# Optimization experiments

Hardware: AMD Instinct MI355X
Metric: run time of the kernel (lower is better)

The kernel has to match this reference:

```python
import jax, jax.numpy as jnp
import numpy as np

N = 25000   # num nodes
E = 500000  # num edges
B = 4       # num queries (batch)
D = 32      # hidden dim
R2 = 474    # doubled num_relation
L = 4       # num conv layers
EPS = 1e-6


def setup_inputs() -> dict:
    key = jax.random.key(0)
    ks = jax.random.split(key, 12)
    return {
        "node_in": jax.random.randint(ks[0], (E,), 0, N),
        "node_out": jax.random.randint(ks[1], (E,), 0, N),
        "relation": jax.random.randint(ks[2], (E,), 0, R2),
        "edge_weight": jnp.ones((E,), jnp.float32),
        "h_index": jax.random.randint(ks[3], (B,), 0, N),
        "r_index": jax.random.randint(ks[4], (B,), 0, R2),
        "query_embed": jax.random.normal(ks[5], (R2, D), jnp.float32) * 0.1,
        "rel_W": jax.random.normal(ks[6], (L, D, R2 * D), jnp.float32) * 0.05,
        "rel_b": jnp.zeros((L, R2 * D), jnp.float32),
        "lin_W": jax.random.normal(ks[7], (L, 13 * D, D), jnp.float32) * 0.05,
        "lin_b": jnp.zeros((L, D), jnp.float32),
        "mlp_W1": jax.random.normal(ks[8], (2 * D, 2 * D), jnp.float32) * 0.05,
        "mlp_b1": jnp.zeros((2 * D,), jnp.float32),
        "mlp_W2": jax.random.normal(ks[9], (2 * D, 1), jnp.float32) * 0.05,
        "mlp_b2": jnp.zeros((1,), jnp.float32),
    }


def _nbfnet(node_in, node_out, relation, h_index, r_index,
            edge_weight, query_embed, rel_W, rel_b, lin_W, lin_b,
            mlp_W1, mlp_b1, mlp_W2, mlp_b2):
    query = query_embed[r_index]                                   # [B, D]
    # boundary condition: query embedding placed at the head node of each query
    boundary = jnp.zeros((N, B, D), query.dtype).at[h_index, jnp.arange(B)].set(query)
    # append one self-entry per node (boundary message), as in the torch code
    node_out_ext = jnp.concatenate([node_out, jnp.arange(N)])      # [E+N]
    w_ext = jnp.concatenate([edge_weight, jnp.ones((N,), edge_weight.dtype)])[:, None, None]
    cnt = jax.ops.segment_sum(jnp.ones((E + N,), query.dtype), node_out_ext, N)[:, None, None]
    deg = jax.ops.segment_sum(edge_weight, node_out, N) + 1.0      # degree_out + 1, [N]
    scale = jnp.log(deg)
    scale = scale / scale.mean()
    scales = jnp.stack([jnp.ones_like(scale), scale, 1.0 / jnp.clip(scale, 0.01)], -1)  # [N,3]

    hidden = boundary
    for l in range(L):
        # dependent relation embeddings: [R2, B, D]
        rel_in = (query @ rel_W[l] + rel_b[l]).reshape(B, R2, D).transpose(1, 0, 2)
        # distmult message + boundary self-message: [E+N, B, D]
        msg = jnp.concatenate([rel_in[relation] * hidden[node_in], boundary], 0)
        mw = msg * w_ext
        mean = jax.ops.segment_sum(mw, node_out_ext, N) / cnt
        sq_mean = jax.ops.segment_sum(msg * mw, node_out_ext, N) / cnt
        mx = jax.ops.segment_max(mw, node_out_ext, N)
        mn = jax.ops.segment_min(mw, node_out_ext, N)
        std = jnp.sqrt(jnp.clip(sq_mean - mean * mean, EPS))
        feat = jnp.stack([mean, mx, mn, std], -1).reshape(N, B, 4 * D)   # PNA stats
        update = (feat[..., None] * scales[:, None, None, :]).reshape(N, B, 12 * D)
        hidden = jax.nn.relu(jnp.concatenate([hidden, update], -1) @ lin_W[l] + lin_b[l])

    feat = jnp.concatenate([hidden, jnp.broadcast_to(query[None], (N, B, D))], -1)  # [N,B,2D]
    h1 = jax.nn.relu(feat @ mlp_W1 + mlp_b1)
    score = (h1 @ mlp_W2 + mlp_b2)[..., 0]                          # [N, B]
    return score.T                                                  # [B, N]


def reference(node_in, node_out, relation, edge_weight, h_index, r_index,
              query_embed, rel_W, rel_b, lin_W, lin_b,
              mlp_W1, mlp_b1, mlp_W2, mlp_b2):
    return _nbfnet(node_in, node_out, relation, h_index, r_index,
                   edge_weight, query_embed, rel_W, rel_b, lin_W, lin_b,
                   mlp_W1, mlp_b1, mlp_W2, mlp_b2)
```

## Files before the change

### kernel.cpp

```cpp
#include <hip/hip_runtime.h>
#include <hip/hip_fp16.h>

#define NN  25000
#define EE  500000
#define BB  4
#define DD  32
#define LL  4
#define R2C 474
#define BD  128
#define THD 416
#define EPSF 1e-6f
#define WMH 13312
#define CAP 64
#define FINF 3.0e38f

#define NEB    245
#define NWMB   208
#define NRELIN 948
#define NW1P   16

typedef _Float16 half8 __attribute__((ext_vector_type(8)));
typedef float    f32x4 __attribute__((ext_vector_type(4)));

__global__ __launch_bounds__(256) void build_setup_kernel(
    const int* __restrict__ node_in, const int* __restrict__ node_out,
    const int* __restrict__ relation, const float* __restrict__ ew,
    int* __restrict__ cnt, int2* __restrict__ ep,
    const float* __restrict__ linW, _Float16* __restrict__ Wm,
    const int* __restrict__ r_index, const float* __restrict__ qemb,
    const float* __restrict__ relW, const float* __restrict__ relB,
    __half* __restrict__ relIn, float* __restrict__ query,
    const float* __restrict__ W1, _Float16* __restrict__ W1m) {
  const int blk = blockIdx.x;
  const int tid = threadIdx.x;
  if (blk < NEB) {
    int i = blk * 256 + tid;
    if (i >= EE / 8) return;
    const int4*   ni4 = (const int4*)node_in;
    const int4*   no4 = (const int4*)node_out;
    const int4*   rl4 = (const int4*)relation;
    const float4* ew4 = (const float4*)ew;
    int4   noA = no4[2 * i], noB = no4[2 * i + 1];
    int4   niA = ni4[2 * i], niB = ni4[2 * i + 1];
    int4   rlA = rl4[2 * i], rlB = rl4[2 * i + 1];
    float4 ewA = ew4[2 * i], ewB = ew4[2 * i + 1];
    int s0 = atomicAdd(&cnt[noA.x], 1);
    int s1 = atomicAdd(&cnt[noA.y], 1);
    int s2 = atomicAdd(&cnt[noA.z], 1);
    int s3 = atomicAdd(&cnt[noA.w], 1);
    int s4 = atomicAdd(&cnt[noB.x], 1);
    int s5 = atomicAdd(&cnt[noB.y], 1);
    int s6 = atomicAdd(&cnt[noB.z], 1);
    int s7 = atomicAdd(&cnt[noB.w], 1);
    ep[noA.x * CAP + s0] = make_int2(niA.x | (rlA.x << 15), __float_as_int(ewA.x));
    ep[noA.y * CAP + s1] = make_int2(niA.y | (rlA.y << 15), __float_as_int(ewA.y));
    ep[noA.z * CAP + s2] = make_int2(niA.z | (rlA.z << 15), __float_as_int(ewA.z));
    ep[noA.w * CAP + s3] = make_int2(niA.w | (rlA.w << 15), __float_as_int(ewA.w));
    ep[noB.x * CAP + s4] = make_int2(niB.x | (rlB.x << 15), __float_as_int(ewB.x));
    ep[noB.y * CAP + s5] = make_int2(niB.y | (rlB.y << 15), __float_as_int(ewB.y));
    ep[noB.z * CAP + s6] = make_int2(niB.z | (rlB.z << 15), __float_as_int(ewB.z));
    ep[noB.w * CAP + s7] = make_int2(niB.w | (rlB.w << 15), __float_as_int(ewB.w));
  } else if (blk < NEB + NWMB) {
    int idx = (blk - NEB) * 256 + tid;
    int l = idx / WMH, rest = idx % WMH;
    int t = rest >> 10;
    int nt = (rest >> 9) & 1;
    int L = (rest >> 3) & 63;
    int j = rest & 7;
    int k = t * 32 + (L >> 4) * 8 + j;
    int n = nt * 16 + (L & 15);
    int wrow;
    if (k < 32) wrow = k;
    else {
      int kk = k - 32;
      int slab = kk >> 7, s = (kk >> 5) & 3, dd = kk & 31;
      wrow = DD + (dd * 4 + s) * 3 + slab;
    }
    Wm[idx] = (_Float16)linW[(size_t)l * THD * DD + (size_t)wrow * DD + n];
  } else if (blk < NEB + NWMB + NRELIN) {
    int o = (blk - NEB - NWMB) * 256 + tid;
    int l = o / (R2C * BD);
    int rest = o % (R2C * BD);
    int r = rest >> 7, b = (rest >> 5) & 3, d = rest & 31;
    int col = r * DD + d;
    const float* W = relW + (size_t)l * DD * R2C * DD;
    const float* qrow = qemb + (size_t)r_index[b] * DD;
    float acc = relB[(size_t)l * R2C * DD + col];
    #pragma unroll
    for (int k = 0; k < DD; ++k)
      acc = fmaf(qrow[k], W[(size_t)k * (R2C * DD) + col], acc);
    relIn[o] = __float2half(acc);
  } else if (blk < NEB + NWMB + NRELIN + NW1P) {
    int idx = (blk - NEB - NWMB - NRELIN) * 256 + tid;
    int kc = idx >> 11;
    int nt = (idx >> 9) & 3;
    int L = (idx >> 3) & 63;
    int j = idx & 7;
    int k = kc * 32 + (L >> 4) * 8 + j;
    int c = nt * 16 + (L & 15);
    W1m[idx] = (_Float16)W1[(size_t)k * (2 * DD) + c];
  } else {
    if (tid < BD) query[tid] = qemb[(size_t)r_index[tid >> 5] * DD + (tid & 31)];
  }
}

__global__ __launch_bounds__(1024) void lg_kernel(const int* __restrict__ cnt,
                                                  const int2* __restrict__ ep,
                                                  float* __restrict__ lg,
                                                  float* __restrict__ logsum) {
  const int lane = threadIdx.x & 63;
  const int wv   = threadIdx.x >> 6;
  const int nb   = blockIdx.x * 256 + wv * 16;
  float acc = 0.f;
  for (int it = 0; it < 16; ++it) {
    int n = nb + it;
    if (n < NN) {
      int c = cnt[n];
      int2 e = ep[(size_t)n * CAP + lane];
      float s = (lane < c) ? __int_as_float(e.y) : 0.f;
      #pragma unroll
      for (int o = 32; o > 0; o >>= 1) s += __shfl_xor(s, o);
      float v = logf(s + 1.0f);
      if (lane == 0) { lg[n] = v; acc += v; }
    }
  }
  __shared__ float red[16];
  if (lane == 0) red[wv] = acc;
  __syncthreads();
  if (threadIdx.x == 0) {
    float t = 0.f;
    #pragma unroll
    for (int i = 0; i < 16; ++i) t += red[i];
    atomicAdd(logsum, t);
  }
}

template <bool LAST>
__device__ __forceinline__ void mfma_epilogue(const _Float16* sh,
                                              const _Float16* hinh,
                                              __half* houth,
                                              const float* lg,
                                              const float* logsum,
                                              const _Float16* Wm,
                                              const float* bias,
                                              const float* query,
                                              const int* h_index,
                                              int nbase, int lane, bool hzero,
                                              const _Float16* W1m,
                                              const float* b1,
                                              const float* W2,
                                              const float* b2,
                                              float* out,
                                              _Float16* hbuf) {
  const int m = lane & 15;
  const int q = lane >> 4;
  const int nl = m >> 2;
  const int n = nbase + nl;
  const int b = m & 3;
  const float sc = lg[n] * ((float)NN / logsum[0]);
  const _Float16 one = (_Float16)1.f;
  const _Float16 s1h = (_Float16)sc;
  const _Float16 s2h = (_Float16)(1.0f / fmaxf(sc, 0.01f));
  const _Float16* ssrc = sh + nl * 512 + b * 32 + q * 8;

  f32x4 c0 = {0.f, 0.f, 0.f, 0.f};
  f32x4 c1 = {0.f, 0.f, 0.f, 0.f};
  half8 a;
  if (hzero) {
    a = (half8)(_Float16)0.f;
    if (n == h_index[b]) {
      const float* qp = query + b * 32 + q * 8;
      #pragma unroll
      for (int j = 0; j < 8; ++j) a[j] = (_Float16)qp[j];
    }
  } else {
    a = *(const half8*)(hinh + (unsigned)n * BD + b * 32 + q * 8);
  }
  #pragma unroll
  for (int t = 0; t < 13; ++t) {
    if (t > 0) {
      const int slab = (t - 1) >> 2, s = (t - 1) & 3;
      a = *(const half8*)(ssrc + s * 128);
      const _Float16 sch = (slab == 0) ? one : ((slab == 1) ? s1h : s2h);
      half8 sv = {sch, sch, sch, sch, sch, sch, sch, sch};
      a = a * sv;
    }
    half8 b0 = *(const half8*)(Wm + (unsigned)(t * 2 + 0) * 512 + lane * 8);
    half8 b1f = *(const half8*)(Wm + (unsigned)(t * 2 + 1) * 512 + lane * 8);
    c0 = __builtin_amdgcn_mfma_f32_16x16x32_f16(a, b0, c0, 0, 0, 0);
    c1 = __builtin_amdgcn_mfma_f32_16x16x32_f16(a, b1f, c1, 0, 0, 0);
  }
  const int col = lane & 15;
  const float bj0 = bias[col], bj1 = bias[col + 16];
  if constexpr (!LAST) {
    #pragma unroll
    for (int i = 0; i < 4; ++i) {
      const int mr = q * 4 + i;
      __half* dst = houth + (unsigned)(nbase + (mr >> 2)) * BD + (mr & 3) * 32 + col;
      dst[0]  = __float2half(fmaxf(c0[i] + bj0, 0.f));
      dst[16] = __float2half(fmaxf(c1[i] + bj1, 0.f));
    }
  } else {
    #pragma unroll
    for (int i = 0; i < 4; ++i) {
      const int mr = q * 4 + i;
      hbuf[mr * 32 + col]      = (_Float16)fmaxf(c0[i] + bj0, 0.f);
      hbuf[mr * 32 + 16 + col] = (_Float16)fmaxf(c1[i] + bj1, 0.f);
    }
    half8 ah = *(const half8*)(hbuf + m * 32 + q * 8);
    half8 aq;
    const float* qp = query + b * 32 + q * 8;
    #pragma unroll
    for (int j = 0; j < 8; ++j) aq[j] = (_Float16)qp[j];
    f32x4 h1c[4];
    #pragma unroll
    for (int nt = 0; nt < 4; ++nt) {
      h1c[nt] = (f32x4){0.f, 0.f, 0.f, 0.f};
      half8 w0 = *(const half8*)(W1m + (unsigned)(0 * 4 + nt) * 512 + lane * 8);
      half8 w1 = *(const half8*)(W1m + (unsigned)(1 * 4 + nt) * 512 + lane * 8);
      h1c[nt] = __builtin_amdgcn_mfma_f32_16x16x32_f16(ah, w0, h1c[nt], 0, 0, 0);
      h1c[nt] = __builtin_amdgcn_mfma_f32_16x16x32_f16(aq, w1, h1c[nt], 0, 0, 0);
    }
    float part[4] = {0.f, 0.f, 0.f, 0.f};
    #pragma unroll
    for (int nt = 0; nt < 4; ++nt) {
      const float bb = b1[nt * 16 + col];
      const float ww = W2[nt * 16 + col];
      #pragma unroll
      for (int i = 0; i < 4; ++i) {
        float v = fmaxf(h1c[nt][i] + bb, 0.f);
        part[i] = fmaf(v, ww, part[i]);
      }
    }
    #pragma unroll
    for (int i = 0; i < 4; ++i) {
      part[i] += __shfl_xor(part[i], 1);
      part[i] += __shfl_xor(part[i], 2);
      part[i] += __shfl_xor(part[i], 4);
      part[i] += __shfl_xor(part[i], 8);
    }
    if (col == 0) {
      const float b2v = b2[0];
      #pragma unroll
      for (int i = 0; i < 4; ++i)
        out[(unsigned)i * NN + nbase + q] = part[i] + b2v;
    }
  }
}

__global__ __launch_bounds__(256) void layer1_fused_kernel(
    const int4* __restrict__ rel4, const int2* __restrict__ ep,
    const int* __restrict__ cnt, const int* __restrict__ h_index,
    const float* __restrict__ query, const float* __restrict__ lg,
    const float* __restrict__ logsum, const _Float16* __restrict__ Wm,
    const float* __restrict__ bias, __half* __restrict__ houth) {
  __shared__ __align__(16) __half2 sh[4][256];
  const int tid = threadIdx.x;
  const int lane = tid & 63;
  const int wid = tid >> 6;
  const int c8 = lane & 15;
  const int eg = lane >> 4;
  const int nbase = blockIdx.x * 4;
  const int n = nbase + wid;
  const int hb = h_index[c8 >> 2];
  const int cnn = __builtin_amdgcn_readfirstlane(cnt[n]);
  const int2 myE = ep[n * CAP + lane];
  const float4* q4 = (const float4*)query;
  float4 qA = q4[c8 * 2], qB = q4[c8 * 2 + 1];
  float q8[8] = {qA.x, qA.y, qA.z, qA.w, qB.x, qB.y, qB.z, qB.w};
  float sa[8], qa[8], mx[8], mn[8];
  const bool g0 = (eg == 0);
  const bool head = (n == hb);
  #pragma unroll
  for (int j = 0; j < 8; ++j) {
    float mv = (g0 && head) ? q8[j] : 0.f;
    sa[j] = mv; qa[j] = mv * mv;
    mx[j] = g0 ? mv : -FINF;
    mn[j] = g0 ? mv : FINF;
  }
  int matched = 0;
  const int nsf = cnn >> 2;
  const int tail = cnn & 3;
  #pragma unroll 2
  for (int j = 0; j < nsf; ++j) {
    int sl = j * 4 + eg;
    int ex = __shfl(myE.x, sl);
    int ey = __shfl(myE.y, sl);
    bool mt = ((ex & 0x7fff) == hb);
    unsigned rr = mt ? ((unsigned)ex >> 15) : 0u;
    float w = mt ? __int_as_float(ey) : 0.f;
    int4 Rv = rel4[rr * 16 + c8];
    const __half2* rp = (const __half2*)&Rv;
    #pragma unroll
    for (int u = 0; u < 4; ++u) {
      float2 rf = __half22float2(rp[u]);
      float m0 = rf.x * q8[2 * u], m1 = rf.y * q8[2 * u + 1];
      float w0 = m0 * w, w1 = m1 * w;
      sa[2 * u] += w0; sa[2 * u + 1] += w1;
      qa[2 * u] = fmaf(m0, w0, qa[2 * u]);
      qa[2 * u + 1] = fmaf(m1, w1, qa[2 * u + 1]);
      mx[2 * u]     = mt ? fmaxf(mx[2 * u], w0)     : mx[2 * u];
      mn[2 * u]     = mt ? fminf(mn[2 * u], w0)     : mn[2 * u];
      mx[2 * u + 1] = mt ? fmaxf(mx[2 * u + 1], w1) : mx[2 * u + 1];
      mn[2 * u + 1] = mt ? fminf(mn[2 * u + 1], w1) : mn[2 * u + 1];
    }
    matched += mt ? 1 : 0;
  }
  if (tail) {
    int sl = nsf * 4 + eg;
    int ex = __shfl(myE.x, sl);
    int ey = __shfl(myE.y, sl);
    bool act = eg < tail;
    bool mt = act && ((ex & 0x7fff) == hb);
    unsigned rr = mt ? ((unsigned)ex >> 15) : 0u;
    float w = mt ? __int_as_float(ey) : 0.f;
    int4 Rv = rel4[rr * 16 + c8];
    const __half2* rp = (const __half2*)&Rv;
    #pragma unroll
    for (int u = 0; u < 4; ++u) {
      float2 rf = __half22float2(rp[u]);
      float m0 = rf.x * q8[2 * u], m1 = rf.y * q8[2 * u + 1];
      float w0 = m0 * w, w1 = m1 * w;
      sa[2 * u] += w0; sa[2 * u + 1] += w1;
      qa[2 * u] = fmaf(m0, w0, qa[2 * u]);
      qa[2 * u + 1] = fmaf(m1, w1, qa[2 * u + 1]);
      mx[2 * u]     = mt ? fmaxf(mx[2 * u], w0)     : mx[2 * u];
      mn[2 * u]     = mt ? fminf(mn[2 * u], w0)     : mn[2 * u];
      mx[2 * u + 1] = mt ? fmaxf(mx[2 * u + 1], w1) : mx[2 * u + 1];
      mn[2 * u + 1] = mt ? fminf(mn[2 * u + 1], w1) : mn[2 * u + 1];
    }
    matched += mt ? 1 : 0;
  }
  #pragma unroll
  for (int j = 0; j < 8; ++j) {
    sa[j] += __shfl_xor(sa[j], 16);
    qa[j] += __shfl_xor(qa[j], 16);
    mx[j] = fmaxf(mx[j], __shfl_xor(mx[j], 16));
    mn[j] = fminf(mn[j], __shfl_xor(mn[j], 16));
    sa[j] += __shfl_xor(sa[j], 32);
    qa[j] += __shfl_xor(qa[j], 32);
    mx[j] = fmaxf(mx[j], __shfl_xor(mx[j], 32));
    mn[j] = fminf(mn[j], __shfl_xor(mn[j], 32));
  }
  matched += __shfl_xor(matched, 16);
  matched += __shfl_xor(matched, 32);
  if (matched < cnn) {
    #pragma unroll
    for (int j = 0; j < 8; ++j) {
      mx[j] = fmaxf(mx[j], 0.f);
      mn[j] = fminf(mn[j], 0.f);
    }
  }
  const float invc = 1.0f / (float)(cnn + 1);
  half8 ov;
  #pragma unroll
  for (int j = 0; j < 8; ++j) {
    float mean = sa[j] * invc;
    float sd = sqrtf(fmaxf(qa[j] * invc - mean * mean, EPSF));
    float v = (eg == 0) ? mean : ((eg == 1) ? mx[j] : ((eg == 2) ? mn[j] : sd));
    ov[j] = (_Float16)v;
  }
  ((half8*)sh)[wid * 64 + eg * 16 + c8] = ov;
  __syncthreads();
  if (tid < 64)
    mfma_epilogue<false>((const _Float16*)&sh[0][0], nullptr, houth, lg, logsum,
                         Wm, bias, query, h_index, nbase, lane, true,
                         nullptr, nullptr, nullptr, nullptr, nullptr, nullptr);
}

template <bool LAST>
__global__ __launch_bounds__(256) void layer_fused_kernel(
    const int4* __restrict__ hin4, const int4* __restrict__ rel4,
    const int2* __restrict__ ep, const int* __restrict__ cnt,
    const int* __restrict__ h_index, const float* __restrict__ query,
    const float* __restrict__ lg, const float* __restrict__ logsum,
    const _Float16* __restrict__ Wm, const float* __restrict__ bias,
    __half* __restrict__ houth,
    const _Float16* __restrict__ W1m, const float* __restrict__ b1,
    const float* __restrict__ W2, const float* __restrict__ b2,
    float* __restrict__ out) {
  __shared__ __align__(16) __half2 sh[4][256];
  __shared__ __align__(16) _Float16 hbuf[512];
  const int tid = threadIdx.x;
  const int lane = tid & 63;
  const int wid = tid >> 6;
  const int c8 = lane & 15;
  const int eg = lane >> 4;
  const int nbase = blockIdx.x * 4;
  const int n = nbase + wid;
  const int hb = h_index[c8 >> 2];
  const int cnn = __builtin_amdgcn_readfirstlane(cnt[n]);
  const int2 myE = ep[n * CAP + lane];
  const float4* q4 = (const float4*)query;
  float4 qA = q4[c8 * 2], qB = q4[c8 * 2 + 1];
  float q8[8] = {qA.x, qA.y, qA.z, qA.w, qB.x, qB.y, qB.z, qB.w};
  float sa[8], qa[8], mx[8], mn[8];
  const bool g0 = (eg == 0);
  const bool head = (n == hb);
  #pragma unroll
  for (int j = 0; j < 8; ++j) {
    float mv = (g0 && head) ? q8[j] : 0.f;
    sa[j] = mv; qa[j] = mv * mv;
    mx[j] = g0 ? mv : -FINF;
    mn[j] = g0 ? mv : FINF;
  }
  const int nsf = cnn >> 2;
  const int tail = cnn & 3;
  #pragma unroll 2
  for (int j = 0; j < nsf; ++j) {
    int sl = j * 4 + eg;
    int ex = __shfl(myE.x, sl);
    int ey = __shfl(myE.y, sl);
    int src = ex & 0x7fff;
    unsigned rr = (unsigned)ex >> 15;
    float w = __int_as_float(ey);
    int4 Hv = hin4[(unsigned)src * 16 + c8];
    int4 Rv = rel4[rr * 16 + c8];
    const __half2* hp = (const __half2*)&Hv;
    const __half2* rp = (const __half2*)&Rv;
    #pragma unroll
    for (int u = 0; u < 4; ++u) {
      float2 hf = __half22float2(hp[u]);
      float2 rf = __half22float2(rp[u]);
      float m0 = rf.x * hf.x, m1 = rf.y * hf.y;
      float w0 = m0 * w, w1 = m1 * w;
      sa[2 * u] += w0; sa[2 * u + 1] += w1;
      qa[2 * u] = fmaf(m0, w0, qa[2 * u]);
      qa[2 * u + 1] = fmaf(m1, w1, qa[2 * u + 1]);
      mx[2 * u] = fmaxf(mx[2 * u], w0);         mn[2 * u] = fminf(mn[2 * u], w0);
      mx[2 * u + 1] = fmaxf(mx[2 * u + 1], w1); mn[2 * u + 1] = fminf(mn[2 * u + 1], w1);
    }
  }
  if (tail) {
    int sl = nsf * 4 + eg;
    int ex = __shfl(myE.x, sl);
    int ey = __shfl(myE.y, sl);
    bool act = eg < tail;
    int src = act ? (ex & 0x7fff) : 0;
    unsigned rr = act ? ((unsigned)ex >> 15) : 0u;
    float w = act ? __int_as_float(ey) : 0.f;
    int4 Hv = hin4[(unsigned)src * 16 + c8];
    int4 Rv = rel4[rr * 16 + c8];
    const __half2* hp = (const __half2*)&Hv;
    const __half2* rp = (const __half2*)&Rv;
    #pragma unroll
    for (int u = 0; u < 4; ++u) {
      float2 hf = __half22float2(hp[u]);
      float2 rf = __half22float2(rp[u]);
      float m0 = rf.x * hf.x, m1 = rf.y * hf.y;
      float w0 = m0 * w, w1 = m1 * w;
      sa[2 * u] += w0; sa[2 * u + 1] += w1;
      qa[2 * u] = fmaf(m0, w0, qa[2 * u]);
      qa[2 * u + 1] = fmaf(m1, w1, qa[2 * u + 1]);
      mx[2 * u]     = act ? fmaxf(mx[2 * u], w0)     : mx[2 * u];
      mn[2 * u]     = act ? fminf(mn[2 * u], w0)     : mn[2 * u];
      mx[2 * u + 1] = act ? fmaxf(mx[2 * u + 1], w1) : mx[2 * u + 1];
      mn[2 * u + 1] = act ? fminf(mn[2 * u + 1], w1) : mn[2 * u + 1];
    }
  }
  #pragma unroll
  for (int j = 0; j < 8; ++j) {
    sa[j] += __shfl_xor(sa[j], 16);
    qa[j] += __shfl_xor(qa[j], 16);
    mx[j] = fmaxf(mx[j], __shfl_xor(mx[j], 16));
    mn[j] = fminf(mn[j], __shfl_xor(mn[j], 16));
    sa[j] += __shfl_xor(sa[j], 32);
    qa[j] += __shfl_xor(qa[j], 32);
    mx[j] = fmaxf(mx[j], __shfl_xor(mx[j], 32));
    mn[j] = fminf(mn[j], __shfl_xor(mn[j], 32));
  }
  const float invc = 1.0f / (float)(cnn + 1);
  half8 ov;
  #pragma unroll
  for (int j = 0; j < 8; ++j) {
    float mean = sa[j] * invc;
    float sd = sqrtf(fmaxf(qa[j] * invc - mean * mean, EPSF));
    float v = (eg == 0) ? mean : ((eg == 1) ? mx[j] : ((eg == 2) ? mn[j] : sd));
    ov[j] = (_Float16)v;
  }
  ((half8*)sh)[wid * 64 + eg * 16 + c8] = ov;
  __syncthreads();
  if (tid < 64)
    mfma_epilogue<LAST>((const _Float16*)&sh[0][0], (const _Float16*)hin4, houth,
                        lg, logsum, Wm, bias, query, h_index, nbase, lane, false,
                        W1m, b1, W2, b2, out, hbuf);
}

extern "C" void kernel_launch(void* const* d_in, const int* in_sizes, int n_in,
                              void* d_out, int out_size, void* d_ws, size_t ws_size,
                              hipStream_t stream) {
  const int*   node_in  = (const int*)d_in[0];
  const int*   node_out = (const int*)d_in[1];
  const int*   relation = (const int*)d_in[2];
  const float* ew       = (const float*)d_in[3];
  const int*   h_index  = (const int*)d_in[4];
  const int*   r_index  = (const int*)d_in[5];
  const float* qemb     = (const float*)d_in[6];
  const float* relW     = (const float*)d_in[7];
  const float* relB     = (const float*)d_in[8];
  const float* linW     = (const float*)d_in[9];
  const float* linB     = (const float*)d_in[10];
  const float* W1       = (const float*)d_in[11];
  const float* b1       = (const float*)d_in[12];
  const float* W2       = (const float*)d_in[13];
  const float* b2       = (const float*)d_in[14];
  float* out = (float*)d_out;

  char* ws = (char*)d_ws;
  size_t off = 0;
  auto alloc = [&](size_t bytes) -> char* {
    char* p = ws + off;
    off += (bytes + 255) & ~(size_t)255;
    return p;
  };
  __half*   h0     = (__half*)  alloc((size_t)NN * BD * 2);
  __half*   h1buf  = (__half*)  alloc((size_t)NN * BD * 2);
  __half*   relIn  = (__half*)  alloc((size_t)LL * R2C * BD * 2);
  _Float16* Wm     = (_Float16*)alloc((size_t)LL * WMH * 2);
  _Float16* W1m    = (_Float16*)alloc((size_t)4096 * 2);
  int2*     ep     = (int2*)    alloc((size_t)NN * CAP * 8);
  int*      cnti   = (int*)     alloc((size_t)NN * 4);
  float*    stats  = (float*)   alloc(256);
  float*    lg     = (float*)   alloc((size_t)NN * 4);
  float*    query  = (float*)   alloc((size_t)BD * 4);

  float* logsum = stats;

  hipMemsetAsync(cnti, 0, (((size_t)NN * 4 + 255) & ~(size_t)255) + 256, stream);

  build_setup_kernel<<<NEB + NWMB + NRELIN + NW1P + 1, 256, 0, stream>>>(
      node_in, node_out, relation, ew, cnti, ep,
      linW, Wm, r_index, qemb, relW, relB, relIn, query, W1, W1m);
  lg_kernel<<<98, 1024, 0, stream>>>(cnti, ep, lg, logsum);

  __half* hin = h0; __half* hout = h1buf;
  for (int l = 0; l < LL; ++l) {
    if (l == 0) {
      layer1_fused_kernel<<<NN / 4, 256, 0, stream>>>(
          (const int4*)relIn, ep, cnti, h_index, query, lg, logsum,
          Wm, linB, hout);
    } else if (l < LL - 1) {
      layer_fused_kernel<false><<<NN / 4, 256, 0, stream>>>(
          (const int4*)hin, (const int4*)relIn + (size_t)l * R2C * 16,
          ep, cnti, h_index, query, lg, logsum,
          Wm + (size_t)l * WMH, linB + (size_t)l * DD, hout,
          nullptr, nullptr, nullptr, nullptr, nullptr);
    } else {
      layer_fused_kernel<true><<<NN / 4, 256, 0, stream>>>(
          (const int4*)hin, (const int4*)relIn + (size_t)l * R2C * 16,
          ep, cnti, h_index, query, lg, logsum,
          Wm + (size_t)l * WMH, linB + (size_t)l * DD, hout,
          W1m, b1, W2, b2, out);
    }
    __half* tmp = hin; hin = hout; hout = tmp;
  }
}
```

Before: 324.4 us.

## Batch edge gathers and switch message max/min to packed fp16 math

The per-node edge loops now issue several hidden-state and relation gathers (5 per batch in general layers, 8 in layer 1) before consuming any of them, so more memory requests are in flight at once. Message products and the max/min accumulators use packed fp16 operations, while the sum and sum-of-squares stay in fp32. The edge-list loads are masked to valid lanes, and launch bounds now request 4 blocks per CU. In layer 1 the matched-edge counting is dropped, because unmatched edges now contribute zero to max/min directly. Risks are fp16 rounding or overflow in the products and higher register pressure from the batched loads.

```diff
diff --git a/kernel.cpp b/kernel.cpp
--- a/kernel.cpp
+++ b/kernel.cpp
@@ -13,6 +13,8 @@
 #define WMH 13312
 #define CAP 64
 #define FINF 3.0e38f
+#define GBATCH 5
+#define L1BATCH 8
 
 #define NEB    245
 #define NWMB   208
@@ -20,7 +22,21 @@
 #define NW1P   16
 
 typedef _Float16 half8 __attribute__((ext_vector_type(8)));
+typedef _Float16 h2v   __attribute__((ext_vector_type(2)));
+typedef float    f2v   __attribute__((ext_vector_type(2)));
 typedef float    f32x4 __attribute__((ext_vector_type(4)));
+
+__device__ __forceinline__ h2v h2max(h2v a, h2v b) {
+  h2v d; asm("v_pk_max_f16 %0, %1, %2" : "=v"(d) : "v"(a), "v"(b)); return d;
+}
+__device__ __forceinline__ h2v h2min(h2v a, h2v b) {
+  h2v d; asm("v_pk_min_f16 %0, %1, %2" : "=v"(d) : "v"(a), "v"(b)); return d;
+}
+__device__ __forceinline__ h2v shflx_h2(h2v v, int m) {
+  union { h2v h; int i; } u; u.h = v;
+  u.i = __shfl_xor(u.i, m);
+  return u.h;
+}
 
 __global__ __launch_bounds__(256) void build_setup_kernel(
     const int* __restrict__ node_in, const int* __restrict__ node_out,
@@ -116,8 +132,9 @@
     int n = nb + it;
     if (n < NN) {
       int c = cnt[n];
-      int2 e = ep[(size_t)n * CAP + lane];
-      float s = (lane < c) ? __int_as_float(e.y) : 0.f;
+      int2 e = make_int2(0, 0);
+      if (lane < c) e = ep[(size_t)n * CAP + lane];
+      float s = __int_as_float(e.y);
       #pragma unroll
       for (int o = 32; o > 0; o >>= 1) s += __shfl_xor(s, o);
       float v = logf(s + 1.0f);
@@ -248,7 +265,41 @@
   }
 }
 
-__global__ __launch_bounds__(256) void layer1_fused_kernel(
+__device__ __forceinline__ void stats_finish(float* sa, float* qa,
+                                             h2v* mx2, h2v* mn2,
+                                             int cnn, int wid, int eg, int c8,
+                                             void* sh) {
+  #pragma unroll
+  for (int j = 0; j < 8; ++j) {
+    sa[j] += __shfl_xor(sa[j], 16);
+    qa[j] += __shfl_xor(qa[j], 16);
+    sa[j] += __shfl_xor(sa[j], 32);
+    qa[j] += __shfl_xor(qa[j], 32);
+  }
+  #pragma unroll
+  for (int u = 0; u < 4; ++u) {
+    mx2[u] = h2max(mx2[u], shflx_h2(mx2[u], 16));
+    mn2[u] = h2min(mn2[u], shflx_h2(mn2[u], 16));
+    mx2[u] = h2max(mx2[u], shflx_h2(mx2[u], 32));
+    mn2[u] = h2min(mn2[u], shflx_h2(mn2[u], 32));
+  }
+  const float invc = 1.0f / (float)(cnn + 1);
+  union { half8 v8; h2v h2[4]; } ov;
+  #pragma unroll
+  for (int u = 0; u < 4; ++u) {
+    float mean0 = sa[2 * u] * invc, mean1 = sa[2 * u + 1] * invc;
+    float sd0 = sqrtf(fmaxf(qa[2 * u] * invc - mean0 * mean0, EPSF));
+    float sd1 = sqrtf(fmaxf(qa[2 * u + 1] * invc - mean1 * mean1, EPSF));
+    h2v mpair = {(_Float16)mean0, (_Float16)mean1};
+    h2v spair = {(_Float16)sd0, (_Float16)sd1};
+    h2v sel = (eg == 0) ? mpair
+            : ((eg == 1) ? mx2[u] : ((eg == 2) ? mn2[u] : spair));
+    ov.h2[u] = sel;
+  }
+  ((half8*)sh)[wid * 64 + eg * 16 + c8] = ov.v8;
+}
+
+__global__ __launch_bounds__(256, 4) void layer1_fused_kernel(
     const int4* __restrict__ rel4, const int2* __restrict__ ep,
     const int* __restrict__ cnt, const int* __restrict__ h_index,
     const float* __restrict__ query, const float* __restrict__ lg,
@@ -264,50 +315,70 @@
   const int n = nbase + wid;
   const int hb = h_index[c8 >> 2];
   const int cnn = __builtin_amdgcn_readfirstlane(cnt[n]);
-  const int2 myE = ep[n * CAP + lane];
+  int2 myE = make_int2(0, 0);
+  if (lane < cnn) myE = ep[n * CAP + lane];
   const float4* q4 = (const float4*)query;
   float4 qA = q4[c8 * 2], qB = q4[c8 * 2 + 1];
   float q8[8] = {qA.x, qA.y, qA.z, qA.w, qB.x, qB.y, qB.z, qB.w};
-  float sa[8], qa[8], mx[8], mn[8];
+  h2v q2h[4];
+  #pragma unroll
+  for (int u = 0; u < 4; ++u)
+    q2h[u] = (h2v){(_Float16)q8[2 * u], (_Float16)q8[2 * u + 1]};
   const bool g0 = (eg == 0);
   const bool head = (n == hb);
+  const _Float16 HI = (_Float16)65504.f;
+  float sa[8], qa[8];
+  h2v mx2[4], mn2[4];
   #pragma unroll
-  for (int j = 0; j < 8; ++j) {
-    float mv = (g0 && head) ? q8[j] : 0.f;
-    sa[j] = mv; qa[j] = mv * mv;
-    mx[j] = g0 ? mv : -FINF;
-    mn[j] = g0 ? mv : FINF;
-  }
-  int matched = 0;
-  const int nsf = cnn >> 2;
+  for (int u = 0; u < 4; ++u) {
+    float mv0 = (g0 && head) ? q8[2 * u] : 0.f;
+    float mv1 = (g0 && head) ? q8[2 * u + 1] : 0.f;
+    sa[2 * u] = mv0; sa[2 * u + 1] = mv1;
+    qa[2 * u] = mv0 * mv0; qa[2 * u + 1] = mv1 * mv1;
+    h2v mvh = {(_Float16)mv0, (_Float16)mv1};
+    mx2[u] = g0 ? mvh : (h2v){-HI, -HI};
+    mn2[u] = g0 ? mvh : (h2v){HI, HI};
+  }
+  const int nf = cnn >> 2;
   const int tail = cnn & 3;
-  #pragma unroll 2
-  for (int j = 0; j < nsf; ++j) {
-    int sl = j * 4 + eg;
-    int ex = __shfl(myE.x, sl);
-    int ey = __shfl(myE.y, sl);
-    bool mt = ((ex & 0x7fff) == hb);
-    unsigned rr = mt ? ((unsigned)ex >> 15) : 0u;
-    float w = mt ? __int_as_float(ey) : 0.f;
-    int4 Rv = rel4[rr * 16 + c8];
-    const __half2* rp = (const __half2*)&Rv;
-    #pragma unroll
-    for (int u = 0; u < 4; ++u) {
-      float2 rf = __half22float2(rp[u]);
-      float m0 = rf.x * q8[2 * u], m1 = rf.y * q8[2 * u + 1];
-      float w0 = m0 * w, w1 = m1 * w;
-      sa[2 * u] += w0; sa[2 * u + 1] += w1;
-      qa[2 * u] = fmaf(m0, w0, qa[2 * u]);
-      qa[2 * u + 1] = fmaf(m1, w1, qa[2 * u + 1]);
-      mx[2 * u]     = mt ? fmaxf(mx[2 * u], w0)     : mx[2 * u];
-      mn[2 * u]     = mt ? fminf(mn[2 * u], w0)     : mn[2 * u];
-      mx[2 * u + 1] = mt ? fmaxf(mx[2 * u + 1], w1) : mx[2 * u + 1];
-      mn[2 * u + 1] = mt ? fminf(mn[2 * u + 1], w1) : mn[2 * u + 1];
-    }
-    matched += mt ? 1 : 0;
+  for (int gbase = 0; gbase < nf; gbase += L1BATCH) {
+    const int gb = min(L1BATCH, nf - gbase);
+    int4 Rv[L1BATCH]; float wv[L1BATCH];
+    #pragma unroll
+    for (int j = 0; j < L1BATCH; ++j) {
+      if (j < gb) {
+        int sl = (gbase + j) * 4 + eg;
+        int ex = __shfl(myE.x, sl);
+        int ey = __shfl(myE.y, sl);
+        bool mt = ((ex & 0x7fff) == hb);
+        unsigned rr = mt ? ((unsigned)ex >> 15) : 0u;
+        wv[j] = mt ? __int_as_float(ey) : 0.f;
+        Rv[j] = rel4[rr * 16 + c8];
+      }
+    }
+    #pragma unroll
+    for (int j = 0; j < L1BATCH; ++j) {
+      if (j < gb) {
+        _Float16 wh = (_Float16)wv[j];
+        h2v w2 = {wh, wh};
+        const h2v* rp = (const h2v*)&Rv[j];
+        #pragma unroll
+        for (int u = 0; u < 4; ++u) {
+          h2v m2 = q2h[u] * rp[u];
+          h2v mw2 = m2 * w2;
+          mx2[u] = h2max(mx2[u], mw2);
+          mn2[u] = h2min(mn2[u], mw2);
+          f2v mf  = __builtin_convertvector(m2, f2v);
+          f2v mwf = __builtin_convertvector(mw2, f2v);
+          sa[2 * u] += mwf[0]; sa[2 * u + 1] += mwf[1];
+          qa[2 * u] = fmaf(mf[0], mwf[0], qa[2 * u]);
+          qa[2 * u + 1] = fmaf(mf[1], mwf[1], qa[2 * u + 1]);
+        }
+      }
+    }
   }
   if (tail) {
-    int sl = nsf * 4 + eg;
+    int sl = (cnn & ~3) + eg;
     int ex = __shfl(myE.x, sl);
     int ey = __shfl(myE.y, sl);
     bool act = eg < tail;
@@ -315,52 +386,25 @@
     unsigned rr = mt ? ((unsigned)ex >> 15) : 0u;
     float w = mt ? __int_as_float(ey) : 0.f;
     int4 Rv = rel4[rr * 16 + c8];
-    const __half2* rp = (const __half2*)&Rv;
+    _Float16 wh = (_Float16)w;
+    h2v w2 = {wh, wh};
+    const h2v* rp = (const h2v*)&Rv;
     #pragma unroll
     for (int u = 0; u < 4; ++u) {
-      float2 rf = __half22float2(rp[u]);
-      float m0 = rf.x * q8[2 * u], m1 = rf.y * q8[2 * u + 1];
-      float w0 = m0 * w, w1 = m1 * w;
-      sa[2 * u] += w0; sa[2 * u + 1] += w1;
-      qa[2 * u] = fmaf(m0, w0, qa[2 * u]);
-      qa[2 * u + 1] = fmaf(m1, w1, qa[2 * u + 1]);
-      mx[2 * u]     = mt ? fmaxf(mx[2 * u], w0)     : mx[2 * u];
-      mn[2 * u]     = mt ? fminf(mn[2 * u], w0)     : mn[2 * u];
-      mx[2 * u + 1] = mt ? fmaxf(mx[2 * u + 1], w1) : mx[2 * u + 1];
-      mn[2 * u + 1] = mt ? fminf(mn[2 * u + 1], w1) : mn[2 * u + 1];
-    }
-    matched += mt ? 1 : 0;
-  }
-  #pragma unroll
-  for (int j = 0; j < 8; ++j) {
-    sa[j] += __shfl_xor(sa[j], 16);
-    qa[j] += __shfl_xor(qa[j], 16);
-    mx[j] = fmaxf(mx[j], __shfl_xor(mx[j], 16));
-    mn[j] = fminf(mn[j], __shfl_xor(mn[j], 16));
-    sa[j] += __shfl_xor(sa[j], 32);
-    qa[j] += __shfl_xor(qa[j], 32);
-    mx[j] = fmaxf(mx[j], __shfl_xor(mx[j], 32));
-    mn[j] = fminf(mn[j], __shfl_xor(mn[j], 32));
-  }
-  matched += __shfl_xor(matched, 16);
-  matched += __shfl_xor(matched, 32);
-  if (matched < cnn) {
-    #pragma unroll
-    for (int j = 0; j < 8; ++j) {
-      mx[j] = fmaxf(mx[j], 0.f);
-      mn[j] = fminf(mn[j], 0.f);
-    }
-  }
-  const float invc = 1.0f / (float)(cnn + 1);
-  half8 ov;
-  #pragma unroll
-  for (int j = 0; j < 8; ++j) {
-    float mean = sa[j] * invc;
-    float sd = sqrtf(fmaxf(qa[j] * invc - mean * mean, EPSF));
-    float v = (eg == 0) ? mean : ((eg == 1) ? mx[j] : ((eg == 2) ? mn[j] : sd));
-    ov[j] = (_Float16)v;
-  }
-  ((half8*)sh)[wid * 64 + eg * 16 + c8] = ov;
+      h2v m2 = q2h[u] * rp[u];
+      h2v mw2 = m2 * w2;
+      if (act) {
+        mx2[u] = h2max(mx2[u], mw2);
+        mn2[u] = h2min(mn2[u], mw2);
+      }
+      f2v mf  = __builtin_convertvector(m2, f2v);
+      f2v mwf = __builtin_convertvector(mw2, f2v);
+      sa[2 * u] += mwf[0]; sa[2 * u + 1] += mwf[1];
+      qa[2 * u] = fmaf(mf[0], mwf[0], qa[2 * u]);
+      qa[2 * u + 1] = fmaf(mf[1], mwf[1], qa[2 * u + 1]);
+    }
+  }
+  stats_finish(sa, qa, mx2, mn2, cnn, wid, eg, c8, (void*)&sh[0][0]);
   __syncthreads();
   if (tid < 64)
     mfma_epilogue<false>((const _Float16*)&sh[0][0], nullptr, houth, lg, logsum,
@@ -369,7 +413,7 @@
 }
 
 template <bool LAST>
-__global__ __launch_bounds__(256) void layer_fused_kernel(
+__global__ __launch_bounds__(256, 4) void layer_fused_kernel(
     const int4* __restrict__ hin4, const int4* __restrict__ rel4,
     const int2* __restrict__ ep, const int* __restrict__ cnt,
     const int* __restrict__ h_index, const float* __restrict__ query,
@@ -390,49 +434,67 @@
   const int n = nbase + wid;
   const int hb = h_index[c8 >> 2];
   const int cnn = __builtin_amdgcn_readfirstlane(cnt[n]);
-  const int2 myE = ep[n * CAP + lane];
+  int2 myE = make_int2(0, 0);
+  if (lane < cnn) myE = ep[n * CAP + lane];
   const float4* q4 = (const float4*)query;
   float4 qA = q4[c8 * 2], qB = q4[c8 * 2 + 1];
   float q8[8] = {qA.x, qA.y, qA.z, qA.w, qB.x, qB.y, qB.z, qB.w};
-  float sa[8], qa[8], mx[8], mn[8];
   const bool g0 = (eg == 0);
   const bool head = (n == hb);
+  const _Float16 HI = (_Float16)65504.f;
+  float sa[8], qa[8];
+  h2v mx2[4], mn2[4];
   #pragma unroll
-  for (int j = 0; j < 8; ++j) {
-    float mv = (g0 && head) ? q8[j] : 0.f;
-    sa[j] = mv; qa[j] = mv * mv;
-    mx[j] = g0 ? mv : -FINF;
-    mn[j] = g0 ? mv : FINF;
-  }
-  const int nsf = cnn >> 2;
+  for (int u = 0; u < 4; ++u) {
+    float mv0 = (g0 && head) ? q8[2 * u] : 0.f;
+    float mv1 = (g0 && head) ? q8[2 * u + 1] : 0.f;
+    sa[2 * u] = mv0; sa[2 * u + 1] = mv1;
+    qa[2 * u] = mv0 * mv0; qa[2 * u + 1] = mv1 * mv1;
+    h2v mvh = {(_Float16)mv0, (_Float16)mv1};
+    mx2[u] = g0 ? mvh : (h2v){-HI, -HI};
+    mn2[u] = g0 ? mvh : (h2v){HI, HI};
+  }
+  const int nf = cnn >> 2;
   const int tail = cnn & 3;
-  #pragma unroll 2
-  for (int j = 0; j < nsf; ++j) {
-    int sl = j * 4 + eg;
-    int ex = __shfl(myE.x, sl);
-    int ey = __shfl(myE.y, sl);
-    int src = ex & 0x7fff;
-    unsigned rr = (unsigned)ex >> 15;
-    float w = __int_as_float(ey);
-    int4 Hv = hin4[(unsigned)src * 16 + c8];
-    int4 Rv = rel4[rr * 16 + c8];
-    const __half2* hp = (const __half2*)&Hv;
-    const __half2* rp = (const __half2*)&Rv;
-    #pragma unroll
-    for (int u = 0; u < 4; ++u) {
-      float2 hf = __half22float2(hp[u]);
-      float2 rf = __half22float2(rp[u]);
-      float m0 = rf.x * hf.x, m1 = rf.y * hf.y;
-      float w0 = m0 * w, w1 = m1 * w;
-      sa[2 * u] += w0; sa[2 * u + 1] += w1;
-      qa[2 * u] = fmaf(m0, w0, qa[2 * u]);
-      qa[2 * u + 1] = fmaf(m1, w1, qa[2 * u + 1]);
-      mx[2 * u] = fmaxf(mx[2 * u], w0);         mn[2 * u] = fminf(mn[2 * u], w0);
-      mx[2 * u + 1] = fmaxf(mx[2 * u + 1], w1); mn[2 * u + 1] = fminf(mn[2 * u + 1], w1);
+  for (int gbase = 0; gbase < nf; gbase += GBATCH) {
+    const int gb = min(GBATCH, nf - gbase);
+    int4 Hv[GBATCH], Rv[GBATCH]; float wv[GBATCH];
+    #pragma unroll
+    for (int j = 0; j < GBATCH; ++j) {
+      if (j < gb) {
+        int sl = (gbase + j) * 4 + eg;
+        int ex = __shfl(myE.x, sl);
+        wv[j] = __int_as_float(__shfl(myE.y, sl));
+        int src = ex & 0x7fff;
+        unsigned rr = (unsigned)ex >> 15;
+        Hv[j] = hin4[(unsigned)src * 16 + c8];
+        Rv[j] = rel4[rr * 16 + c8];
+      }
+    }
+    #pragma unroll
+    for (int j = 0; j < GBATCH; ++j) {
+      if (j < gb) {
+        _Float16 wh = (_Float16)wv[j];
+        h2v w2 = {wh, wh};
+        const h2v* hp = (const h2v*)&Hv[j];
+        const h2v* rp = (const h2v*)&Rv[j];
+        #pragma unroll
+        for (int u = 0; u < 4; ++u) {
+          h2v m2 = hp[u] * rp[u];
+          h2v mw2 = m2 * w2;
+          mx2[u] = h2max(mx2[u], mw2);
+          mn2[u] = h2min(mn2[u], mw2);
+          f2v mf  = __builtin_convertvector(m2, f2v);
+          f2v mwf = __builtin_convertvector(mw2, f2v);
+          sa[2 * u] += mwf[0]; sa[2 * u + 1] += mwf[1];
+          qa[2 * u] = fmaf(mf[0], mwf[0], qa[2 * u]);
+          qa[2 * u + 1] = fmaf(mf[1], mwf[1], qa[2 * u + 1]);
+        }
+      }
     }
   }
   if (tail) {
-    int sl = nsf * 4 + eg;
+    int sl = (cnn & ~3) + eg;
     int ex = __shfl(myE.x, sl);
     int ey = __shfl(myE.y, sl);
     bool act = eg < tail;
@@ -441,44 +503,26 @@
     float w = act ? __int_as_float(ey) : 0.f;
     int4 Hv = hin4[(unsigned)src * 16 + c8];
     int4 Rv = rel4[rr * 16 + c8];
-    const __half2* hp = (const __half2*)&Hv;
-    const __half2* rp = (const __half2*)&Rv;
+    _Float16 wh = (_Float16)w;
+    h2v w2 = {wh, wh};
+    const h2v* hp = (const h2v*)&Hv;
+    const h2v* rp = (const h2v*)&Rv;
     #pragma unroll
     for (int u = 0; u < 4; ++u) {
-      float2 hf = __half22float2(hp[u]);
-      float2 rf = __half22float2(rp[u]);
-      float m0 = rf.x * hf.x, m1 = rf.y * hf.y;
-      float w0 = m0 * w, w1 = m1 * w;
-      sa[2 * u] += w0; sa[2 * u + 1] += w1;
-      qa[2 * u] = fmaf(m0, w0, qa[2 * u]);
-      qa[2 * u + 1] = fmaf(m1, w1, qa[2 * u + 1]);
-      mx[2 * u]     = act ? fmaxf(mx[2 * u], w0)     : mx[2 * u];
-      mn[2 * u]     = act ? fminf(mn[2 * u], w0)     : mn[2 * u];
-      mx[2 * u + 1] = act ? fmaxf(mx[2 * u + 1], w1) : mx[2 * u + 1];
-      mn[2 * u + 1] = act ? fminf(mn[2 * u + 1], w1) : mn[2 * u + 1];
-    }
-  }
-  #pragma unroll
-  for (int j = 0; j < 8; ++j) {
-    sa[j] += __shfl_xor(sa[j], 16);
-    qa[j] += __shfl_xor(qa[j], 16);
-    mx[j] = fmaxf(mx[j], __shfl_xor(mx[j], 16));
-    mn[j] = fminf(mn[j], __shfl_xor(mn[j], 16));
-    sa[j] += __shfl_xor(sa[j], 32);
-    qa[j] += __shfl_xor(qa[j], 32);
-    mx[j] = fmaxf(mx[j], __shfl_xor(mx[j], 32));
-    mn[j] = fminf(mn[j], __shfl_xor(mn[j], 32));
-  }
-  const float invc = 1.0f / (float)(cnn + 1);
-  half8 ov;
-  #pragma unroll
-  for (int j = 0; j < 8; ++j) {
-    float mean = sa[j] * invc;
-    float sd = sqrtf(fmaxf(qa[j] * invc - mean * mean, EPSF));
-    float v = (eg == 0) ? mean : ((eg == 1) ? mx[j] : ((eg == 2) ? mn[j] : sd));
-    ov[j] = (_Float16)v;
-  }
-  ((half8*)sh)[wid * 64 + eg * 16 + c8] = ov;
+      h2v m2 = hp[u] * rp[u];
+      h2v mw2 = m2 * w2;
+      if (act) {
+        mx2[u] = h2max(mx2[u], mw2);
+        mn2[u] = h2min(mn2[u], mw2);
+      }
+      f2v mf  = __builtin_convertvector(m2, f2v);
+      f2v mwf = __builtin_convertvector(mw2, f2v);
+      sa[2 * u] += mwf[0]; sa[2 * u + 1] += mwf[1];
+      qa[2 * u] = fmaf(mf[0], mwf[0], qa[2 * u]);
+      qa[2 * u + 1] = fmaf(mf[1], mwf[1], qa[2 * u + 1]);
+    }
+  }
+  stats_finish(sa, qa, mx2, mn2, cnn, wid, eg, c8, (void*)&sh[0][0]);
   __syncthreads();
   if (tid < 64)
     mfma_epilogue<LAST>((const _Float16*)&sh[0][0], (const _Float16*)hin4, houth,
```

After: 292.0 us. -10.0%, faster.
